# Kernel optimization log

Hardware: AMD Instinct MI355X
Metric: run time of the kernel (lower is better)

The kernel has to match this reference:

```python
import math
import jax, jax.numpy as jnp
import numpy as np

INF = 10000000000.0
B, S, D = 4, 4096, 64


def setup_inputs() -> dict:
    key = jax.random.key(0)
    kq, kk, kv = jax.random.split(key, 3)
    query = jax.random.normal(kq, (B, S, D), dtype=jnp.float32)
    k = jax.random.normal(kk, (B, S, D), dtype=jnp.float32)
    value = jax.random.normal(kv, (B, S, D), dtype=jnp.float32)
    padding = jnp.zeros((B, S), dtype=bool)  # True = masked-out key position
    return {"query": query, "key": k, "value": value, "padding": padding}


def reference(query, key, value, padding):
    # Faithful to torch Attention.forward with causal=True, dropout=0.
    scale = math.sqrt(query.shape[-1])  # sqrt(d_key)
    # [B, Sq, Sk] scores
    dot = jnp.einsum("bqd,bkd->bqk", query, key)
    Sk = key.shape[1]
    # causal: subtract INF on strict upper triangle (applied BEFORE scaling, as in source)
    tri = jnp.triu(jnp.ones((Sk, Sk), dtype=dot.dtype), 1) * INF
    dot = dot - tri[None, :, :]
    # padding mask: set masked key columns to -INF
    dot = jnp.where(padding[:, None, :], -INF, dot)
    probs = jax.nn.softmax(dot / scale, axis=-1)
    return jnp.einsum("bqk,bkd->bqd", probs, value)
```

## Files before the change

kernel.cpp:

```cpp
#include <hip/hip_runtime.h>
#include <hip/hip_bf16.h>


#define S_LEN 4096
#define D_DIM 64
#define NBATCH 4
#define QBLK 128
#define KVBLK 64
#define NQB (S_LEN / QBLK)
#define SLOT_B 17408

typedef __attribute__((ext_vector_type(16))) float f32x16;
typedef __attribute__((ext_vector_type(4))) float f32x4;
typedef __attribute__((ext_vector_type(8))) short s16x8;
typedef __attribute__((ext_vector_type(4))) short s16x4;
typedef __attribute__((ext_vector_type(2))) unsigned int u32x2;

#define FK(n) ((((n) ^ ((n) >> 3)) & 7) << 4)
#define FV(d) (((((d) & 7) << 4)) ^ ((((d) >> 3) & 1) << 3))

__device__ __forceinline__ unsigned short f2bfu(float f) {
  return __builtin_bit_cast(unsigned short, __float2bfloat16(f));
}
__device__ __forceinline__ unsigned pk2(float a, float b) {
  return (unsigned)f2bfu(a) | ((unsigned)f2bfu(b) << 16);
}
__device__ __forceinline__ float bf2f(short s) {
  return __builtin_bit_cast(float, ((unsigned)(unsigned short)s) << 16);
}

__global__ __launch_bounds__(256, 3) void fattn_partial(
    const float* __restrict__ Qg, const float* __restrict__ Kg,
    const float* __restrict__ Vg, const unsigned char* __restrict__ Pad,
    char* __restrict__ Ws, int CL, int TOTC)
{
  const int wid = blockIdx.x;
  const int b   = wid & 3;
  const int u   = TOTC - 1 - (wid >> 2);
  int Qb = 0, ci = 0;
  {
    int uu = u, q = 0;
    while (true) {
      const int nch = (2 * q + 2 + CL - 1) / CL;
      if (uu < nch) { ci = uu; break; }
      uu -= nch; ++q;
    }
    Qb = q;
  }
  const int q0  = Qb * QBLK;
  const int ntt = 2 * Qb + 2;
  const int t0  = ci * CL;
  const int t1  = (t0 + CL < ntt) ? (t0 + CL) : ntt;

  const int tid = threadIdx.x;
  const int w   = tid >> 6;
  const int l   = tid & 63;
  const int ql  = l & 31;
  const int hi  = l >> 5;
  const int qw0 = q0 + 32 * w;
  const int qa  = qw0 + ql;

  const int sq  = l & 3;
  const int sm  = (l >> 2) & 3;
  const int sc2 = l >> 4;
  const int snb = 4 * w + 16 * sc2;

  __shared__ short Ksh[KVBLK * D_DIM];
  __shared__ short Vtsh[D_DIM * KVBLK];
  __shared__ int anyPadSh;

  const unsigned char* PadB = Pad + (size_t)b * S_LEN;

  if (tid == 0) anyPadSh = 0;
  __syncthreads();
  {
    const int nk  = (t1 - t0) * KVBLK;
    const int idx = 2 * tid;
    if (idx < nk) {
      const unsigned char* pp = PadB + t0 * KVBLK + idx;
      const bool nz = pp[0] || ((idx + 1 < nk) ? pp[1] : (unsigned char)0);
      if (nz) anyPadSh = 1;
    }
  }

  s16x8 qf[4];
  {
    const float* qp = Qg + ((size_t)(b * S_LEN + qa)) * D_DIM + 8 * hi;
    #pragma unroll
    for (int dc = 0; dc < 4; ++dc)
      #pragma unroll
      for (int j = 0; j < 8; ++j)
        qf[dc][j] = (short)f2bfu(qp[16 * dc + j] * 0.125f);
  }

  f32x16 acc[2];
  #pragma unroll
  for (int dt = 0; dt < 2; ++dt)
    #pragma unroll
    for (int i = 0; i < 16; ++i) acc[dt][i] = 0.f;
  float mrow = -INFINITY;
  float lrow = 0.f;

  u32x2 kpb[4], vpb[4];

#define LOAD_KV(T) do {                                                      \
    const int kv0_ = (T) * KVBLK;                                            \
    _Pragma("unroll")                                                        \
    for (int s_ = 0; s_ < 4; ++s_) {                                         \
      const size_t go_ =                                                     \
          ((size_t)(b * S_LEN + kv0_ + snb + sq)) * D_DIM + 16 * s_ + 4 * sm;\
      const float4 kx = *(const float4*)(Kg + go_);                          \
      const float4 vx = *(const float4*)(Vg + go_);                          \
      kpb[s_][0] = pk2(kx.x, kx.y); kpb[s_][1] = pk2(kx.z, kx.w);            \
      vpb[s_][0] = pk2(vx.x, vx.y); vpb[s_][1] = pk2(vx.z, vx.w);            \
    }                                                                        \
  } while (0)

#define STAGE() do {                                                         \
    _Pragma("unroll")                                                        \
    for (int s_ = 0; s_ < 4; ++s_) {                                         \
      const int d0_ = 16 * s_ + 4 * sm; const int nk_ = snb + sq;            \
      *(u32x2*)((char*)&Ksh[0] + nk_ * 128 + ((2 * d0_) ^ FK(nk_))) =        \
          kpb[s_];                                                           \
      unsigned u0 = vpb[s_][0], u1 = vpb[s_][1];                             \
      unsigned x_ = (sq & 2) ? u0 : u1;                                      \
      unsigned y_ = __shfl_xor(x_, 2);                                       \
      unsigned A0 = (sq & 2) ? y_ : u0;                                      \
      unsigned A1 = (sq & 2) ? u1 : y_;                                      \
      unsigned z0 = __shfl_xor(A0, 1);                                       \
      unsigned z1 = __shfl_xor(A1, 1);                                       \
      unsigned o0, o1;                                                       \
      if (sq & 1) { o0 = (z0 >> 16) | (A0 & 0xFFFF0000u);                    \
                    o1 = (z1 >> 16) | (A1 & 0xFFFF0000u); }                  \
      else        { o0 = (A0 & 0xFFFFu) | (z0 << 16);                        \
                    o1 = (A1 & 0xFFFFu) | (z1 << 16); }                      \
      const int dv_ = d0_ + sq;                                              \
      u32x2 vv2; vv2[0] = o0; vv2[1] = o1;                                   \
      *(u32x2*)((char*)&Vtsh[0] + dv_ * 128 + ((2 * snb) ^ FV(dv_))) = vv2;  \
    }                                                                        \
  } while (0)

  LOAD_KV(t0);

  for (int t = t0; t < t1; ++t) {
    STAGE();
    __syncthreads();
    const bool more = (t + 1 < t1);
    if (more) LOAD_KV(t + 1);

    const int kv0 = t * KVBLK;

    f32x16 sv[2];
    __builtin_amdgcn_s_setprio(1);
    #pragma unroll
    for (int kt = 0; kt < 2; ++kt) {
      f32x16 a;
      #pragma unroll
      for (int i = 0; i < 16; ++i) a[i] = 0.f;
      #pragma unroll
      for (int dc = 0; dc < 4; ++dc) {
        const int nr = 32 * kt + ql;
        const s16x8 kf = *(const s16x8*)((char*)&Ksh[0] + nr * 128 +
                                         ((32 * dc + 16 * hi) ^ FK(nr)));
        a = __builtin_amdgcn_mfma_f32_32x32x16_bf16(kf, qf[dc], a, 0, 0, 0);
      }
      sv[kt] = a;
    }
    __builtin_amdgcn_s_setprio(0);

    if (anyPadSh) {
      #pragma unroll
      for (int kt = 0; kt < 2; ++kt)
        #pragma unroll
        for (int r1 = 0; r1 < 4; ++r1) {
          const unsigned pd =
              *(const unsigned*)(PadB + kv0 + 32 * kt + 8 * r1 + 4 * hi);
          #pragma unroll
          for (int r0 = 0; r0 < 4; ++r0)
            if ((pd >> (8 * r0)) & 0xFFu) sv[kt][4 * r1 + r0] = -1e30f;
        }
    }
    #pragma unroll
    for (int kt = 0; kt < 2; ++kt) {
      const int kvt = kv0 + 32 * kt;
      if (kvt + 31 > qw0) {
        #pragma unroll
        for (int r1 = 0; r1 < 4; ++r1)
          #pragma unroll
          for (int r0 = 0; r0 < 4; ++r0)
            if (kvt + 8 * r1 + 4 * hi + r0 > qa) sv[kt][4 * r1 + r0] = -1e30f;
      }
    }

    f32x16 mx;
    #pragma unroll
    for (int i = 0; i < 16; ++i) mx[i] = fmaxf(sv[0][i], sv[1][i]);
    f32x4 m4;
    #pragma unroll
    for (int i = 0; i < 4; ++i)
      m4[i] = fmaxf(fmaxf(mx[i], mx[i + 4]), fmaxf(mx[i + 8], mx[i + 12]));
    float vm = fmaxf(fmaxf(m4[0], m4[1]), fmaxf(m4[2], m4[3]));
    vm = fmaxf(vm, __shfl_xor(vm, 32));
    const float mn   = fmaxf(mrow, vm);
    const float corr = __expf(mrow - mn);
    mrow = mn;
    lrow *= corr;
    #pragma unroll
    for (int dt = 0; dt < 2; ++dt)
      #pragma unroll
      for (int i = 0; i < 16; ++i) acc[dt][i] *= corr;

    float rs0 = 0.f, rs1 = 0.f, rs2 = 0.f, rs3 = 0.f;
    #pragma unroll
    for (int kt = 0; kt < 2; ++kt)
      #pragma unroll
      for (int i4 = 0; i4 < 16; i4 += 4) {
        const float p0 = __expf(sv[kt][i4 + 0] - mn);
        const float p1 = __expf(sv[kt][i4 + 1] - mn);
        const float p2 = __expf(sv[kt][i4 + 2] - mn);
        const float p3 = __expf(sv[kt][i4 + 3] - mn);
        sv[kt][i4 + 0] = p0; sv[kt][i4 + 1] = p1;
        sv[kt][i4 + 2] = p2; sv[kt][i4 + 3] = p3;
        rs0 += p0; rs1 += p1; rs2 += p2; rs3 += p3;
      }
    lrow += (rs0 + rs1) + (rs2 + rs3);

    __builtin_amdgcn_s_setprio(1);
    #pragma unroll
    for (int sk = 0; sk < 4; ++sk) {
      const int kt = sk >> 1, rb = 8 * (sk & 1);
      union { unsigned u[4]; s16x8 v; } pb;
      pb.u[0] = pk2(sv[kt][rb + 0], sv[kt][rb + 1]);
      pb.u[1] = pk2(sv[kt][rb + 2], sv[kt][rb + 3]);
      pb.u[2] = pk2(sv[kt][rb + 4], sv[kt][rb + 5]);
      pb.u[3] = pk2(sv[kt][rb + 6], sv[kt][rb + 7]);
      #pragma unroll
      for (int dt = 0; dt < 2; ++dt) {
        const int dr = 32 * dt + ql;
        const char* vrow = (char*)&Vtsh[0] + dr * 128;
        const s16x4 v0 = *(const s16x4*)(vrow + ((32 * sk + 8 * hi) ^ FV(dr)));
        const s16x4 v1 = *(const s16x4*)(vrow + ((32 * sk + 16 + 8 * hi) ^ FV(dr)));
        s16x8 vf;
        vf[0] = v0[0]; vf[1] = v0[1]; vf[2] = v0[2]; vf[3] = v0[3];
        vf[4] = v1[0]; vf[5] = v1[1]; vf[6] = v1[2]; vf[7] = v1[3];
        acc[dt] = __builtin_amdgcn_mfma_f32_32x32x16_bf16(vf, pb.v, acc[dt], 0, 0, 0);
      }
    }
    __builtin_amdgcn_s_setprio(0);

    __syncthreads();
  }

  const float lt = lrow + __shfl_xor(lrow, 32);

  char* slot = Ws + ((size_t)b * TOTC + u) * SLOT_B;
  const int row = 32 * w + ql;
  #pragma unroll
  for (int dt = 0; dt < 2; ++dt)
    #pragma unroll
    for (int r1 = 0; r1 < 4; ++r1) {
      u32x2 p;
      p[0] = pk2(acc[dt][4 * r1 + 0], acc[dt][4 * r1 + 1]);
      p[1] = pk2(acc[dt][4 * r1 + 2], acc[dt][4 * r1 + 3]);
      *(u32x2*)(slot + row * 128 + (32 * dt + 8 * r1 + 4 * hi) * 2) = p;
    }
  if (hi == 0) {
    ((float*)(slot + 16384))[row]       = mrow;
    ((float*)(slot + 16384 + 512))[row] = lt;
  }
}

__global__ __launch_bounds__(256, 8) void fattn_merge(
    const char* __restrict__ Ws, float* __restrict__ Og, int CL, int TOTC)
{
  const int blk = blockIdx.x;
  const int qbi = blk >> 2;
  const int qr  = blk & 3;
  const int Qb  = qbi & (NQB - 1);
  const int b   = qbi >> 5;
  const int tid = threadIdx.x;
  const int row = 32 * qr + (tid >> 3);
  const int d0  = (tid & 7) * 8;

  const int ntt    = 2 * Qb + 2;
  const int nvalid = (ntt + CL - 1) / CL;
  int pre = 0;
  for (int q = 0; q < Qb; ++q) pre += (2 * q + 2 + CL - 1) / CL;

  const char* base = Ws + ((size_t)b * TOTC + pre) * SLOT_B;

  float mstar = -INFINITY;
  for (int ci = 0; ci < nvalid; ++ci)
    mstar = fmaxf(mstar, ((const float*)(base + (size_t)ci * SLOT_B + 16384))[row]);

  float lsum = 0.f;
  float o[8];
  #pragma unroll
  for (int k = 0; k < 8; ++k) o[k] = 0.f;

  for (int ci = 0; ci < nvalid; ++ci) {
    const char* slot = base + (size_t)ci * SLOT_B;
    const float wgt = __expf(((const float*)(slot + 16384))[row] - mstar);
    lsum += wgt * ((const float*)(slot + 16384 + 512))[row];
    const s16x8 ov = *(const s16x8*)(slot + row * 128 + d0 * 2);
    #pragma unroll
    for (int k = 0; k < 8; ++k) o[k] += wgt * bf2f(ov[k]);
  }

  const float inv = 1.0f / lsum;
  float* op = Og + ((size_t)(b * S_LEN + Qb * QBLK + row)) * D_DIM + d0;
  f32x4 o0, o1;
  #pragma unroll
  for (int k = 0; k < 4; ++k) { o0[k] = o[k] * inv; o1[k] = o[4 + k] * inv; }
  *(f32x4*)(op) = o0;
  *(f32x4*)(op + 4) = o1;
}

extern "C" void kernel_launch(void* const* d_in, const int* in_sizes, int n_in,
                              void* d_out, int out_size, void* d_ws, size_t ws_size,
                              hipStream_t stream) {
  const float* Q = (const float*)d_in[0];
  const float* K = (const float*)d_in[1];
  const float* V = (const float*)d_in[2];
  const unsigned char* P = (const unsigned char*)d_in[3];
  float* O  = (float*)d_out;
  char*  Ws = (char*)d_ws;

  int CL = 4;
  int TOTC = 0;
  for (int q = 0; q < NQB; ++q) TOTC += (2 * q + 2 + CL - 1) / CL;
  if (ws_size < (size_t)NBATCH * TOTC * SLOT_B) {
    CL = 8;
    TOTC = 0;
    for (int q = 0; q < NQB; ++q) TOTC += (2 * q + 2 + CL - 1) / CL;
  }

  dim3 grid(NBATCH * TOTC);
  dim3 block(256);
  hipLaunchKernelGGL(fattn_partial, grid, block, 0, stream, Q, K, V, P, Ws,
                     CL, TOTC);
  hipLaunchKernelGGL(fattn_merge, dim3(NBATCH * NQB * 4), dim3(256), 0, stream,
                     Ws, O, CL, TOTC);
}
```

Before: 59.04 us.

## Switch to single-wave blocks over 32-row query tiles without barriers

Each block now holds one 64-thread wavefront handling a 32-row query tile, in place of four waves sharing a 128-row tile. Each wave loads, converts and transposes its own K/V tile into LDS directly. This drops the register prefetch, the shuffle-based transpose and all __syncthreads, and checks padding with a wave ballot. The aim is to remove barrier stalls and give finer causal work granularity. In exchange, K/V global traffic and conversion work rise roughly fourfold because each wave refetches tiles the old block shared, and load latency is no longer overlapped by prefetch.

```diff
diff --git a/kernel.cpp b/kernel.cpp
--- a/kernel.cpp
+++ b/kernel.cpp
@@ -5,10 +5,9 @@
 #define S_LEN 4096
 #define D_DIM 64
 #define NBATCH 4
-#define QBLK 128
 #define KVBLK 64
-#define NQB (S_LEN / QBLK)
-#define SLOT_B 17408
+#define NQW 128
+#define SLOT_B 4352
 
 typedef __attribute__((ext_vector_type(16))) float f32x16;
 typedef __attribute__((ext_vector_type(4))) float f32x4;
@@ -29,7 +28,7 @@
   return __builtin_bit_cast(float, ((unsigned)(unsigned short)s) << 16);
 }
 
-__global__ __launch_bounds__(256, 3) void fattn_partial(
+__global__ __launch_bounds__(64, 3) void fattn_partial(
     const float* __restrict__ Qg, const float* __restrict__ Kg,
     const float* __restrict__ Vg, const unsigned char* __restrict__ Pad,
     char* __restrict__ Ws, int CL, int TOTC)
@@ -37,55 +36,52 @@
   const int wid = blockIdx.x;
   const int b   = wid & 3;
   const int u   = TOTC - 1 - (wid >> 2);
-  int Qb = 0, ci = 0;
+  int qb = 0, ci = 0;
   {
     int uu = u, q = 0;
     while (true) {
-      const int nch = (2 * q + 2 + CL - 1) / CL;
+      const int nt_  = (q + 2) >> 1;
+      const int nch = (nt_ + CL - 1) / CL;
       if (uu < nch) { ci = uu; break; }
       uu -= nch; ++q;
     }
-    Qb = q;
-  }
-  const int q0  = Qb * QBLK;
-  const int ntt = 2 * Qb + 2;
+    qb = q;
+  }
+  const int qw0 = 32 * qb;
+  const int nt  = (qb + 2) >> 1;
   const int t0  = ci * CL;
-  const int t1  = (t0 + CL < ntt) ? (t0 + CL) : ntt;
-
-  const int tid = threadIdx.x;
-  const int w   = tid >> 6;
-  const int l   = tid & 63;
+  const int t1  = (t0 + CL < nt) ? (t0 + CL) : nt;
+
+  const int l   = threadIdx.x;
   const int ql  = l & 31;
   const int hi  = l >> 5;
-  const int qw0 = q0 + 32 * w;
   const int qa  = qw0 + ql;
 
-  const int sq  = l & 3;
-  const int sm  = (l >> 2) & 3;
-  const int sc2 = l >> 4;
-  const int snb = 4 * w + 16 * sc2;
+  const int krow = l >> 2;
+  const int kd0  = (l & 3) << 4;
+  const int vn0  = (l & 15) << 2;
+  const int vdg  = l >> 4;
 
   __shared__ short Ksh[KVBLK * D_DIM];
   __shared__ short Vtsh[D_DIM * KVBLK];
-  __shared__ int anyPadSh;
-
-  const unsigned char* PadB = Pad + (size_t)b * S_LEN;
-
-  if (tid == 0) anyPadSh = 0;
-  __syncthreads();
+
+  const size_t bS = (size_t)b * S_LEN;
+  const unsigned char* PadB = Pad + bS;
+
+  bool anyPad;
   {
-    const int nk  = (t1 - t0) * KVBLK;
-    const int idx = 2 * tid;
-    if (idx < nk) {
-      const unsigned char* pp = PadB + t0 * KVBLK + idx;
-      const bool nz = pp[0] || ((idx + 1 < nk) ? pp[1] : (unsigned char)0);
-      if (nz) anyPadSh = 1;
-    }
+    const int nk = (t1 - t0) * KVBLK;
+    bool nz = false;
+    if (8 * l < nk) {
+      const unsigned* pp = (const unsigned*)(PadB + t0 * KVBLK + 8 * l);
+      nz = (pp[0] | pp[1]) != 0u;
+    }
+    anyPad = (__ballot(nz) != 0ull);
   }
 
   s16x8 qf[4];
   {
-    const float* qp = Qg + ((size_t)(b * S_LEN + qa)) * D_DIM + 8 * hi;
+    const float* qp = Qg + (bS + qa) * D_DIM + 8 * hi;
     #pragma unroll
     for (int dc = 0; dc < 4; ++dc)
       #pragma unroll
@@ -101,54 +97,42 @@
   float mrow = -INFINITY;
   float lrow = 0.f;
 
-  u32x2 kpb[4], vpb[4];
-
-#define LOAD_KV(T) do {                                                      \
-    const int kv0_ = (T) * KVBLK;                                            \
-    _Pragma("unroll")                                                        \
-    for (int s_ = 0; s_ < 4; ++s_) {                                         \
-      const size_t go_ =                                                     \
-          ((size_t)(b * S_LEN + kv0_ + snb + sq)) * D_DIM + 16 * s_ + 4 * sm;\
-      const float4 kx = *(const float4*)(Kg + go_);                          \
-      const float4 vx = *(const float4*)(Vg + go_);                          \
-      kpb[s_][0] = pk2(kx.x, kx.y); kpb[s_][1] = pk2(kx.z, kx.w);            \
-      vpb[s_][0] = pk2(vx.x, vx.y); vpb[s_][1] = pk2(vx.z, vx.w);            \
-    }                                                                        \
-  } while (0)
-
-#define STAGE() do {                                                         \
-    _Pragma("unroll")                                                        \
-    for (int s_ = 0; s_ < 4; ++s_) {                                         \
-      const int d0_ = 16 * s_ + 4 * sm; const int nk_ = snb + sq;            \
-      *(u32x2*)((char*)&Ksh[0] + nk_ * 128 + ((2 * d0_) ^ FK(nk_))) =        \
-          kpb[s_];                                                           \
-      unsigned u0 = vpb[s_][0], u1 = vpb[s_][1];                             \
-      unsigned x_ = (sq & 2) ? u0 : u1;                                      \
-      unsigned y_ = __shfl_xor(x_, 2);                                       \
-      unsigned A0 = (sq & 2) ? y_ : u0;                                      \
-      unsigned A1 = (sq & 2) ? u1 : y_;                                      \
-      unsigned z0 = __shfl_xor(A0, 1);                                       \
-      unsigned z1 = __shfl_xor(A1, 1);                                       \
-      unsigned o0, o1;                                                       \
-      if (sq & 1) { o0 = (z0 >> 16) | (A0 & 0xFFFF0000u);                    \
-                    o1 = (z1 >> 16) | (A1 & 0xFFFF0000u); }                  \
-      else        { o0 = (A0 & 0xFFFFu) | (z0 << 16);                        \
-                    o1 = (A1 & 0xFFFFu) | (z1 << 16); }                      \
-      const int dv_ = d0_ + sq;                                              \
-      u32x2 vv2; vv2[0] = o0; vv2[1] = o1;                                   \
-      *(u32x2*)((char*)&Vtsh[0] + dv_ * 128 + ((2 * snb) ^ FV(dv_))) = vv2;  \
-    }                                                                        \
-  } while (0)
-
-  LOAD_KV(t0);
-
   for (int t = t0; t < t1; ++t) {
-    STAGE();
-    __syncthreads();
-    const bool more = (t + 1 < t1);
-    if (more) LOAD_KV(t + 1);
-
     const int kv0 = t * KVBLK;
+
+    #pragma unroll
+    for (int i = 0; i < 4; ++i) {
+      const int nk = krow + 16 * i;
+      const float* kp = Kg + (bS + kv0 + nk) * D_DIM + kd0;
+      char* rowp = (char*)Ksh + nk * 128;
+      #pragma unroll
+      for (int j = 0; j < 4; ++j) {
+        const float4 kx = *(const float4*)(kp + 4 * j);
+        u32x2 kb;
+        kb[0] = pk2(kx.x, kx.y); kb[1] = pk2(kx.z, kx.w);
+        *(u32x2*)(rowp + ((2 * (kd0 + 4 * j)) ^ FK(nk))) = kb;
+      }
+    }
+    #pragma unroll
+    for (int i = 0; i < 4; ++i) {
+      const int d0v = 4 * (vdg + 4 * i);
+      const float* vp = Vg + (bS + kv0 + vn0) * D_DIM + d0v;
+      const float4 r0 = *(const float4*)(vp);
+      const float4 r1 = *(const float4*)(vp + D_DIM);
+      const float4 r2 = *(const float4*)(vp + 2 * D_DIM);
+      const float4 r3 = *(const float4*)(vp + 3 * D_DIM);
+      const float* f0 = (const float*)&r0;
+      const float* f1 = (const float*)&r1;
+      const float* f2 = (const float*)&r2;
+      const float* f3 = (const float*)&r3;
+      #pragma unroll
+      for (int j = 0; j < 4; ++j) {
+        const int d = d0v + j;
+        u32x2 p;
+        p[0] = pk2(f0[j], f1[j]); p[1] = pk2(f2[j], f3[j]);
+        *(u32x2*)((char*)Vtsh + d * 128 + ((2 * vn0) ^ FV(d))) = p;
+      }
+    }
 
     f32x16 sv[2];
     __builtin_amdgcn_s_setprio(1);
@@ -160,7 +144,7 @@
       #pragma unroll
       for (int dc = 0; dc < 4; ++dc) {
         const int nr = 32 * kt + ql;
-        const s16x8 kf = *(const s16x8*)((char*)&Ksh[0] + nr * 128 +
+        const s16x8 kf = *(const s16x8*)((char*)Ksh + nr * 128 +
                                          ((32 * dc + 16 * hi) ^ FK(nr)));
         a = __builtin_amdgcn_mfma_f32_32x32x16_bf16(kf, qf[dc], a, 0, 0, 0);
       }
@@ -168,7 +152,7 @@
     }
     __builtin_amdgcn_s_setprio(0);
 
-    if (anyPadSh) {
+    if (anyPad) {
       #pragma unroll
       for (int kt = 0; kt < 2; ++kt)
         #pragma unroll
@@ -237,7 +221,7 @@
       #pragma unroll
       for (int dt = 0; dt < 2; ++dt) {
         const int dr = 32 * dt + ql;
-        const char* vrow = (char*)&Vtsh[0] + dr * 128;
+        const char* vrow = (char*)Vtsh + dr * 128;
         const s16x4 v0 = *(const s16x4*)(vrow + ((32 * sk + 8 * hi) ^ FV(dr)));
         const s16x4 v1 = *(const s16x4*)(vrow + ((32 * sk + 16 + 8 * hi) ^ FV(dr)));
         s16x8 vf;
@@ -247,14 +231,11 @@
       }
     }
     __builtin_amdgcn_s_setprio(0);
-
-    __syncthreads();
   }
 
   const float lt = lrow + __shfl_xor(lrow, 32);
 
   char* slot = Ws + ((size_t)b * TOTC + u) * SLOT_B;
-  const int row = 32 * w + ql;
   #pragma unroll
   for (int dt = 0; dt < 2; ++dt)
     #pragma unroll
@@ -262,11 +243,11 @@
       u32x2 p;
       p[0] = pk2(acc[dt][4 * r1 + 0], acc[dt][4 * r1 + 1]);
       p[1] = pk2(acc[dt][4 * r1 + 2], acc[dt][4 * r1 + 3]);
-      *(u32x2*)(slot + row * 128 + (32 * dt + 8 * r1 + 4 * hi) * 2) = p;
+      *(u32x2*)(slot + ql * 128 + (32 * dt + 8 * r1 + 4 * hi) * 2) = p;
     }
   if (hi == 0) {
-    ((float*)(slot + 16384))[row]       = mrow;
-    ((float*)(slot + 16384 + 512))[row] = lt;
+    ((float*)(slot + 4096))[ql]       = mrow;
+    ((float*)(slot + 4096 + 128))[ql] = lt;
   }
 }
 
@@ -274,24 +255,22 @@
     const char* __restrict__ Ws, float* __restrict__ Og, int CL, int TOTC)
 {
   const int blk = blockIdx.x;
-  const int qbi = blk >> 2;
-  const int qr  = blk & 3;
-  const int Qb  = qbi & (NQB - 1);
-  const int b   = qbi >> 5;
+  const int b   = blk >> 7;
+  const int qb  = blk & 127;
   const int tid = threadIdx.x;
-  const int row = 32 * qr + (tid >> 3);
+  const int row = tid >> 3;
   const int d0  = (tid & 7) * 8;
 
-  const int ntt    = 2 * Qb + 2;
-  const int nvalid = (ntt + CL - 1) / CL;
+  const int nt     = (qb + 2) >> 1;
+  const int nvalid = (nt + CL - 1) / CL;
   int pre = 0;
-  for (int q = 0; q < Qb; ++q) pre += (2 * q + 2 + CL - 1) / CL;
+  for (int q = 0; q < qb; ++q) pre += (((q + 2) >> 1) + CL - 1) / CL;
 
   const char* base = Ws + ((size_t)b * TOTC + pre) * SLOT_B;
 
   float mstar = -INFINITY;
   for (int ci = 0; ci < nvalid; ++ci)
-    mstar = fmaxf(mstar, ((const float*)(base + (size_t)ci * SLOT_B + 16384))[row]);
+    mstar = fmaxf(mstar, ((const float*)(base + (size_t)ci * SLOT_B + 4096))[row]);
 
   float lsum = 0.f;
   float o[8];
@@ -300,15 +279,15 @@
 
   for (int ci = 0; ci < nvalid; ++ci) {
     const char* slot = base + (size_t)ci * SLOT_B;
-    const float wgt = __expf(((const float*)(slot + 16384))[row] - mstar);
-    lsum += wgt * ((const float*)(slot + 16384 + 512))[row];
+    const float wgt = __expf(((const float*)(slot + 4096))[row] - mstar);
+    lsum += wgt * ((const float*)(slot + 4096 + 128))[row];
     const s16x8 ov = *(const s16x8*)(slot + row * 128 + d0 * 2);
     #pragma unroll
     for (int k = 0; k < 8; ++k) o[k] += wgt * bf2f(ov[k]);
   }
 
   const float inv = 1.0f / lsum;
-  float* op = Og + ((size_t)(b * S_LEN + Qb * QBLK + row)) * D_DIM + d0;
+  float* op = Og + ((size_t)(b * S_LEN + 32 * qb + row)) * D_DIM + d0;
   f32x4 o0, o1;
   #pragma unroll
   for (int k = 0; k < 4; ++k) { o0[k] = o[k] * inv; o1[k] = o[4 + k] * inv; }
@@ -328,17 +307,15 @@
 
   int CL = 4;
   int TOTC = 0;
-  for (int q = 0; q < NQB; ++q) TOTC += (2 * q + 2 + CL - 1) / CL;
+  for (int q = 0; q < NQW; ++q) TOTC += (((q + 2) >> 1) + CL - 1) / CL;
   if (ws_size < (size_t)NBATCH * TOTC * SLOT_B) {
     CL = 8;
     TOTC = 0;
-    for (int q = 0; q < NQB; ++q) TOTC += (2 * q + 2 + CL - 1) / CL;
-  }
-
-  dim3 grid(NBATCH * TOTC);
-  dim3 block(256);
-  hipLaunchKernelGGL(fattn_partial, grid, block, 0, stream, Q, K, V, P, Ws,
-                     CL, TOTC);
-  hipLaunchKernelGGL(fattn_merge, dim3(NBATCH * NQB * 4), dim3(256), 0, stream,
+    for (int q = 0; q < NQW; ++q) TOTC += (((q + 2) >> 1) + CL - 1) / CL;
+  }
+
+  hipLaunchKernelGGL(fattn_partial, dim3(NBATCH * TOTC), dim3(64), 0, stream,
+                     Q, K, V, P, Ws, CL, TOTC);
+  hipLaunchKernelGGL(fattn_merge, dim3(NBATCH * NQW), dim3(256), 0, stream,
                      Ws, O, CL, TOTC);
 }
```

After: 91.59 us. 55.1% more time.

## Load V transposed directly and process softmax per 32-key subtile

Applied to the files above, without the earlier changes.

V staging now has each thread load four consecutive rows of four dims and pack bf16 pairs along the key axis. This writes the transposed Vt tile to LDS without the shuffle-based transpose. The inner loop is also split so scores, online softmax and PV MMAs run per 32-key half instead of over the full 64-key block. That lowers register pressure, but it doubles the max, rescale and exp-correction overhead per tile and adds a serial dependency between the halves.

```diff
diff --git a/kernel.cpp b/kernel.cpp
--- a/kernel.cpp
+++ b/kernel.cpp
@@ -64,12 +64,15 @@
   const int sm  = (l >> 2) & 3;
   const int sc2 = l >> 4;
   const int snb = 4 * w + 16 * sc2;
+  const int vn0 = (tid & 15) << 2;
+  const int vd0 = (tid >> 4) << 2;
 
   __shared__ short Ksh[KVBLK * D_DIM];
   __shared__ short Vtsh[D_DIM * KVBLK];
   __shared__ int anyPadSh;
 
-  const unsigned char* PadB = Pad + (size_t)b * S_LEN;
+  const size_t bS = (size_t)b * S_LEN;
+  const unsigned char* PadB = Pad + bS;
 
   if (tid == 0) anyPadSh = 0;
   __syncthreads();
@@ -85,7 +88,7 @@
 
   s16x8 qf[4];
   {
-    const float* qp = Qg + ((size_t)(b * S_LEN + qa)) * D_DIM + 8 * hi;
+    const float* qp = Qg + (bS + qa) * D_DIM + 8 * hi;
     #pragma unroll
     for (int dc = 0; dc < 4; ++dc)
       #pragma unroll
@@ -108,11 +111,21 @@
     _Pragma("unroll")                                                        \
     for (int s_ = 0; s_ < 4; ++s_) {                                         \
       const size_t go_ =                                                     \
-          ((size_t)(b * S_LEN + kv0_ + snb + sq)) * D_DIM + 16 * s_ + 4 * sm;\
+          (bS + kv0_ + snb + sq) * D_DIM + 16 * s_ + 4 * sm;                 \
       const float4 kx = *(const float4*)(Kg + go_);                          \
-      const float4 vx = *(const float4*)(Vg + go_);                          \
       kpb[s_][0] = pk2(kx.x, kx.y); kpb[s_][1] = pk2(kx.z, kx.w);            \
-      vpb[s_][0] = pk2(vx.x, vx.y); vpb[s_][1] = pk2(vx.z, vx.w);            \
+    }                                                                        \
+    const float* vp_ = Vg + (bS + kv0_ + vn0) * D_DIM + vd0;                 \
+    const float4 r0 = *(const float4*)(vp_);                                 \
+    const float4 r1 = *(const float4*)(vp_ + D_DIM);                         \
+    const float4 r2 = *(const float4*)(vp_ + 2 * D_DIM);                     \
+    const float4 r3 = *(const float4*)(vp_ + 3 * D_DIM);                     \
+    const float* f0 = (const float*)&r0; const float* f1 = (const float*)&r1;\
+    const float* f2 = (const float*)&r2; const float* f3 = (const float*)&r3;\
+    _Pragma("unroll")                                                        \
+    for (int j_ = 0; j_ < 4; ++j_) {                                         \
+      vpb[j_][0] = pk2(f0[j_], f1[j_]);                                      \
+      vpb[j_][1] = pk2(f2[j_], f3[j_]);                                      \
     }                                                                        \
   } while (0)
 
@@ -122,21 +135,9 @@
       const int d0_ = 16 * s_ + 4 * sm; const int nk_ = snb + sq;            \
       *(u32x2*)((char*)&Ksh[0] + nk_ * 128 + ((2 * d0_) ^ FK(nk_))) =        \
           kpb[s_];                                                           \
-      unsigned u0 = vpb[s_][0], u1 = vpb[s_][1];                             \
-      unsigned x_ = (sq & 2) ? u0 : u1;                                      \
-      unsigned y_ = __shfl_xor(x_, 2);                                       \
-      unsigned A0 = (sq & 2) ? y_ : u0;                                      \
-      unsigned A1 = (sq & 2) ? u1 : y_;                                      \
-      unsigned z0 = __shfl_xor(A0, 1);                                       \
-      unsigned z1 = __shfl_xor(A1, 1);                                       \
-      unsigned o0, o1;                                                       \
-      if (sq & 1) { o0 = (z0 >> 16) | (A0 & 0xFFFF0000u);                    \
-                    o1 = (z1 >> 16) | (A1 & 0xFFFF0000u); }                  \
-      else        { o0 = (A0 & 0xFFFFu) | (z0 << 16);                        \
-                    o1 = (A1 & 0xFFFFu) | (z1 << 16); }                      \
-      const int dv_ = d0_ + sq;                                              \
-      u32x2 vv2; vv2[0] = o0; vv2[1] = o1;                                   \
-      *(u32x2*)((char*)&Vtsh[0] + dv_ * 128 + ((2 * snb) ^ FV(dv_))) = vv2;  \
+      const int dv_ = vd0 + s_;                                              \
+      *(u32x2*)((char*)&Vtsh[0] + dv_ * 128 + ((2 * vn0) ^ FV(dv_))) =       \
+          vpb[s_];                                                           \
     }                                                                        \
   } while (0)
 
@@ -150,103 +151,96 @@
 
     const int kv0 = t * KVBLK;
 
-    f32x16 sv[2];
-    __builtin_amdgcn_s_setprio(1);
     #pragma unroll
     for (int kt = 0; kt < 2; ++kt) {
-      f32x16 a;
-      #pragma unroll
-      for (int i = 0; i < 16; ++i) a[i] = 0.f;
-      #pragma unroll
-      for (int dc = 0; dc < 4; ++dc) {
-        const int nr = 32 * kt + ql;
-        const s16x8 kf = *(const s16x8*)((char*)&Ksh[0] + nr * 128 +
-                                         ((32 * dc + 16 * hi) ^ FK(nr)));
-        a = __builtin_amdgcn_mfma_f32_32x32x16_bf16(kf, qf[dc], a, 0, 0, 0);
-      }
-      sv[kt] = a;
-    }
-    __builtin_amdgcn_s_setprio(0);
-
-    if (anyPadSh) {
-      #pragma unroll
-      for (int kt = 0; kt < 2; ++kt)
+      f32x16 sv;
+      __builtin_amdgcn_s_setprio(1);
+      {
+        f32x16 a;
+        #pragma unroll
+        for (int i = 0; i < 16; ++i) a[i] = 0.f;
+        #pragma unroll
+        for (int dc = 0; dc < 4; ++dc) {
+          const int nr = 32 * kt + ql;
+          const s16x8 kf = *(const s16x8*)((char*)&Ksh[0] + nr * 128 +
+                                           ((32 * dc + 16 * hi) ^ FK(nr)));
+          a = __builtin_amdgcn_mfma_f32_32x32x16_bf16(kf, qf[dc], a, 0, 0, 0);
+        }
+        sv = a;
+      }
+      __builtin_amdgcn_s_setprio(0);
+
+      const int kvt = kv0 + 32 * kt;
+      if (anyPadSh) {
         #pragma unroll
         for (int r1 = 0; r1 < 4; ++r1) {
           const unsigned pd =
-              *(const unsigned*)(PadB + kv0 + 32 * kt + 8 * r1 + 4 * hi);
+              *(const unsigned*)(PadB + kvt + 8 * r1 + 4 * hi);
           #pragma unroll
           for (int r0 = 0; r0 < 4; ++r0)
-            if ((pd >> (8 * r0)) & 0xFFu) sv[kt][4 * r1 + r0] = -1e30f;
+            if ((pd >> (8 * r0)) & 0xFFu) sv[4 * r1 + r0] = -1e30f;
         }
-    }
-    #pragma unroll
-    for (int kt = 0; kt < 2; ++kt) {
-      const int kvt = kv0 + 32 * kt;
+      }
       if (kvt + 31 > qw0) {
         #pragma unroll
         for (int r1 = 0; r1 < 4; ++r1)
           #pragma unroll
           for (int r0 = 0; r0 < 4; ++r0)
-            if (kvt + 8 * r1 + 4 * hi + r0 > qa) sv[kt][4 * r1 + r0] = -1e30f;
-      }
+            if (kvt + 8 * r1 + 4 * hi + r0 > qa) sv[4 * r1 + r0] = -1e30f;
+      }
+
+      f32x4 m4;
+      #pragma unroll
+      for (int i = 0; i < 4; ++i)
+        m4[i] = fmaxf(fmaxf(sv[i], sv[i + 4]), fmaxf(sv[i + 8], sv[i + 12]));
+      float vm = fmaxf(fmaxf(m4[0], m4[1]), fmaxf(m4[2], m4[3]));
+      vm = fmaxf(vm, __shfl_xor(vm, 32));
+      const float mn   = fmaxf(mrow, vm);
+      const float corr = __expf(mrow - mn);
+      mrow = mn;
+      lrow *= corr;
+      #pragma unroll
+      for (int dt = 0; dt < 2; ++dt)
+        #pragma unroll
+        for (int i = 0; i < 16; ++i) acc[dt][i] *= corr;
+
+      float rs0 = 0.f, rs1 = 0.f, rs2 = 0.f, rs3 = 0.f;
+      #pragma unroll
+      for (int i4 = 0; i4 < 16; i4 += 4) {
+        const float p0 = __expf(sv[i4 + 0] - mn);
+        const float p1 = __expf(sv[i4 + 1] - mn);
+        const float p2 = __expf(sv[i4 + 2] - mn);
+        const float p3 = __expf(sv[i4 + 3] - mn);
+        sv[i4 + 0] = p0; sv[i4 + 1] = p1;
+        sv[i4 + 2] = p2; sv[i4 + 3] = p3;
+        rs0 += p0; rs1 += p1; rs2 += p2; rs3 += p3;
+      }
+      lrow += (rs0 + rs1) + (rs2 + rs3);
+
+      __builtin_amdgcn_s_setprio(1);
+      #pragma unroll
+      for (int sh = 0; sh < 2; ++sh) {
+        const int sk = 2 * kt + sh;
+        const int rb = 8 * sh;
+        union { unsigned uu[4]; s16x8 v; } pb;
+        pb.uu[0] = pk2(sv[rb + 0], sv[rb + 1]);
+        pb.uu[1] = pk2(sv[rb + 2], sv[rb + 3]);
+        pb.uu[2] = pk2(sv[rb + 4], sv[rb + 5]);
+        pb.uu[3] = pk2(sv[rb + 6], sv[rb + 7]);
+        #pragma unroll
+        for (int dt = 0; dt < 2; ++dt) {
+          const int dr = 32 * dt + ql;
+          const char* vrow = (char*)&Vtsh[0] + dr * 128;
+          const s16x4 v0 = *(const s16x4*)(vrow + ((32 * sk + 8 * hi) ^ FV(dr)));
+          const s16x4 v1 = *(const s16x4*)(vrow + ((32 * sk + 16 + 8 * hi) ^ FV(dr)));
+          s16x8 vf;
+          vf[0] = v0[0]; vf[1] = v0[1]; vf[2] = v0[2]; vf[3] = v0[3];
+          vf[4] = v1[0]; vf[5] = v1[1]; vf[6] = v1[2]; vf[7] = v1[3];
+          acc[dt] = __builtin_amdgcn_mfma_f32_32x32x16_bf16(vf, pb.v, acc[dt], 0, 0, 0);
+        }
+      }
+      __builtin_amdgcn_s_setprio(0);
     }
-
-    f32x16 mx;
-    #pragma unroll
-    for (int i = 0; i < 16; ++i) mx[i] = fmaxf(sv[0][i], sv[1][i]);
-    f32x4 m4;
-    #pragma unroll
-    for (int i = 0; i < 4; ++i)
-      m4[i] = fmaxf(fmaxf(mx[i], mx[i + 4]), fmaxf(mx[i + 8], mx[i + 12]));
-    float vm = fmaxf(fmaxf(m4[0], m4[1]), fmaxf(m4[2], m4[3]));
-    vm = fmaxf(vm, __shfl_xor(vm, 32));
-    const float mn   = fmaxf(mrow, vm);
-    const float corr = __expf(mrow - mn);
-    mrow = mn;
-    lrow *= corr;
-    #pragma unroll
-    for (int dt = 0; dt < 2; ++dt)
-      #pragma unroll
-      for (int i = 0; i < 16; ++i) acc[dt][i] *= corr;
-
-    float rs0 = 0.f, rs1 = 0.f, rs2 = 0.f, rs3 = 0.f;
-    #pragma unroll
-    for (int kt = 0; kt < 2; ++kt)
-      #pragma unroll
-      for (int i4 = 0; i4 < 16; i4 += 4) {
-        const float p0 = __expf(sv[kt][i4 + 0] - mn);
-        const float p1 = __expf(sv[kt][i4 + 1] - mn);
-        const float p2 = __expf(sv[kt][i4 + 2] - mn);
-        const float p3 = __expf(sv[kt][i4 + 3] - mn);
-        sv[kt][i4 + 0] = p0; sv[kt][i4 + 1] = p1;
-        sv[kt][i4 + 2] = p2; sv[kt][i4 + 3] = p3;
-        rs0 += p0; rs1 += p1; rs2 += p2; rs3 += p3;
-      }
-    lrow += (rs0 + rs1) + (rs2 + rs3);
-
-    __builtin_amdgcn_s_setprio(1);
-    #pragma unroll
-    for (int sk = 0; sk < 4; ++sk) {
-      const int kt = sk >> 1, rb = 8 * (sk & 1);
-      union { unsigned u[4]; s16x8 v; } pb;
-      pb.u[0] = pk2(sv[kt][rb + 0], sv[kt][rb + 1]);
-      pb.u[1] = pk2(sv[kt][rb + 2], sv[kt][rb + 3]);
-      pb.u[2] = pk2(sv[kt][rb + 4], sv[kt][rb + 5]);
-      pb.u[3] = pk2(sv[kt][rb + 6], sv[kt][rb + 7]);
-      #pragma unroll
-      for (int dt = 0; dt < 2; ++dt) {
-        const int dr = 32 * dt + ql;
-        const char* vrow = (char*)&Vtsh[0] + dr * 128;
-        const s16x4 v0 = *(const s16x4*)(vrow + ((32 * sk + 8 * hi) ^ FV(dr)));
-        const s16x4 v1 = *(const s16x4*)(vrow + ((32 * sk + 16 + 8 * hi) ^ FV(dr)));
-        s16x8 vf;
-        vf[0] = v0[0]; vf[1] = v0[1]; vf[2] = v0[2]; vf[3] = v0[3];
-        vf[4] = v1[0]; vf[5] = v1[1]; vf[6] = v1[2]; vf[7] = v1[3];
-        acc[dt] = __builtin_amdgcn_mfma_f32_32x32x16_bf16(vf, pb.v, acc[dt], 0, 0, 0);
-      }
-    }
-    __builtin_amdgcn_s_setprio(0);
 
     __syncthreads();
   }
```

Result: faster. 56.05 us (-5.1%).
